# Kernel optimization log

Measured on AMD Instinct MI355X. Metric: run time of the kernel, lower is better.

## Reference

```python
import jax, jax.numpy as jnp
import numpy as np

REG_MAX = 16
NC = 80
TOPK = 10
ALPHA = 1.0
BETA = 6.0
BOX_W, CLS_W, DFL_W = 7.5, 0.5, 1.5
IMG = 1280.0


def _ciou(b1, b2, eps=1e-7):
    # b1, b2: [..., 4] xyxy, broadcastable
    b1x1, b1y1, b1x2, b1y2 = b1[..., 0], b1[..., 1], b1[..., 2], b1[..., 3]
    b2x1, b2y1, b2x2, b2y2 = b2[..., 0], b2[..., 1], b2[..., 2], b2[..., 3]
    w1, h1 = b1x2 - b1x1, b1y2 - b1y1
    w2, h2 = b2x2 - b2x1, b2y2 - b2y1
    inter = (jnp.maximum(jnp.minimum(b1x2, b2x2) - jnp.maximum(b1x1, b2x1), 0.0) *
             jnp.maximum(jnp.minimum(b1y2, b2y2) - jnp.maximum(b1y1, b2y1), 0.0))
    union = w1 * h1 + w2 * h2 - inter + eps
    iou = inter / union
    cw = jnp.maximum(b1x2, b2x2) - jnp.minimum(b1x1, b2x1)
    ch = jnp.maximum(b1y2, b2y2) - jnp.minimum(b1y1, b2y1)
    c2 = cw * cw + ch * ch + eps
    rho2 = ((b2x1 + b2x2 - b1x1 - b1x2) ** 2 + (b2y1 + b2y2 - b1y1 - b1y2) ** 2) / 4.0
    v = (4.0 / np.pi ** 2) * (jnp.arctan(w2 / (h2 + eps)) - jnp.arctan(w1 / (h1 + eps))) ** 2
    alpha = jax.lax.stop_gradient(v / (v - iou + (1.0 + eps)))
    return iou - (rho2 / c2 + v * alpha)


def _loss(p0, p1, p2, gt_boxes, gt_labels, strides):
    preds = [p0, p1, p2]
    B = p0.shape[0]
    aps, sts, pds, pcs = [], [], [], []
    for i, p in enumerate(preds):
        H, W = p.shape[2], p.shape[3]
        gy, gx = jnp.meshgrid(jnp.arange(H, dtype=p.dtype) + 0.5,
                              jnp.arange(W, dtype=p.dtype) + 0.5, indexing='ij')
        aps.append(jnp.stack([gx.ravel(), gy.ravel()], -1))          # [HW,2] feat units
        sts.append(jnp.ones((H * W, 1), p.dtype) * strides[i])       # [HW,1]
        pds.append(p[:, :4 * REG_MAX].reshape(B, 4, REG_MAX, H * W).transpose(0, 3, 1, 2))
        pcs.append(p[:, 4 * REG_MAX:].transpose(0, 2, 3, 1).reshape(B, H * W, NC))
    ap = jnp.concatenate(aps)                 # [N,2]
    st = jnp.concatenate(sts)                 # [N,1]
    pred_dist = jnp.concatenate(pds, axis=1)  # [B,N,4,R]
    pred_cls = jnp.concatenate(pcs, axis=1)   # [B,N,NC]
    proj = jnp.arange(REG_MAX, dtype=p0.dtype)
    M = gt_boxes.shape[1]
    N = ap.shape[0]

    def one_image(pd, pc, gb, gl):
        # decode boxes (image units)
        dist = jnp.einsum('nkr,r->nk', jax.nn.softmax(pd, -1), proj)        # [N,4]
        pred_boxes = jnp.concatenate([(ap - dist[:, :2]) * st,
                                      (ap + dist[:, 2:]) * st], -1)          # [N,4]
        # ---- TaskAlignedAssigner (no grad) ----
        sg = jax.lax.stop_gradient
        pb, ps, gbs = sg(pred_boxes), sg(jax.nn.sigmoid(pc)), sg(gb)
        ap_img = ap * st                                                     # [N,2]
        in_gt = ((ap_img[:, None, 0] >= gbs[None, :, 0]) & (ap_img[:, None, 0] <= gbs[None, :, 2]) &
                 (ap_img[:, None, 1] >= gbs[None, :, 1]) & (ap_img[:, None, 1] <= gbs[None, :, 3]))
        ious = jnp.maximum(_ciou(pb[:, None, :], gbs[None, :, :]), 0.0)      # [N,M]
        align = (ps[:, gl] ** ALPHA) * (ious ** BETA) * in_gt
        align = align / (align.max(0, keepdims=True) + 1e-9)
        align = align * (ious > 0.1)
        # topk anchors per GT; anchor takes the GT with max masked score
        #  sequential loop with strict '>' updates)
        vals, idx = jax.lax.top_k(align.T, TOPK)                             # [M,TOPK]
        masked = jnp.zeros((M, N), align.dtype).at[
            jnp.arange(M)[:, None], idx].set(jnp.where(vals > 0, vals, 0.0))
        col = masked.T                                                       # [N,M]
        best_gt = jnp.argmax(col, 1)
        best_score = col.max(1)
        fg = (best_score > 0).astype(pd.dtype)                               # [N]
        num_fg = jnp.maximum(fg.sum(), 1.0)
        labels = gl[best_gt]
        boxes = gbs[best_gt]
        # ---- box (CIoU) loss over fg ----
        box_loss = ((1.0 - _ciou(pred_boxes, boxes)) * fg).sum() / num_fg
        # ---- DFL loss over fg ----
        t = jnp.concatenate([ap - boxes[:, :2] / st, boxes[:, 2:] / st - ap], -1)
        t = jnp.clip(t, 0.0, REG_MAX - 1 - 0.01)   # box2dist clamp
        t = jnp.clip(t, 0.0, REG_MAX - 1e-4)       # DFLLoss clamp
        left = jnp.floor(t).astype(jnp.int32)
        right = jnp.minimum(left + 1, REG_MAX - 1)
        wl = right.astype(t.dtype) - t
        wr = t - left.astype(t.dtype)
        logp = jax.nn.log_softmax(pd, -1)                                    # [N,4,R]
        ce_l = -jnp.take_along_axis(logp, left[..., None], -1)[..., 0]
        ce_r = -jnp.take_along_axis(logp, right[..., None], -1)[..., 0]
        dfl_loss = ((ce_l * wl + ce_r * wr) * fg[:, None]).sum() / (num_fg * 4.0)
        # ---- cls BCE-with-logits over all anchors ----
        cls_t = jax.nn.one_hot(labels, NC, dtype=pc.dtype) * (best_score * fg)[:, None]
        cls_loss = (jnp.logaddexp(0.0, pc) - pc * cls_t).sum(1).mean()
        has_fg = (fg.sum() > 0).astype(pd.dtype)
        return box_loss * has_fg, cls_loss * has_fg, dfl_loss * has_fg

    bl, cl, dl = jax.vmap(one_image)(pred_dist, pred_cls, gt_boxes, gt_labels)
    return BOX_W * bl.sum() + CLS_W * cl.sum() + DFL_W * dl.sum()


def setup_inputs() -> dict:
    key = jax.random.key(0)
    ks = jax.random.split(key, 6)
    p0 = jax.random.normal(ks[0], (8, 144, 160, 160), jnp.float32)
    p1 = jax.random.normal(ks[1], (8, 144, 80, 80), jnp.float32)
    p2 = jax.random.normal(ks[2], (8, 144, 40, 40), jnp.float32)
    cxcy = jax.random.uniform(ks[3], (8, 32, 2), minval=64.0, maxval=IMG - 64.0)
    wh = jax.random.uniform(ks[4], (8, 32, 2), minval=16.0, maxval=256.0)
    gt_boxes = jnp.clip(jnp.concatenate([cxcy - wh / 2, cxcy + wh / 2], -1), 0.0, IMG)
    gt_labels = jax.random.randint(ks[5], (8, 32), 0, NC)
    strides = jnp.array([8.0, 16.0, 32.0], jnp.float32)
    return {"p0": p0, "p1": p1, "p2": p2, "gt_boxes": gt_boxes,
            "gt_labels": gt_labels, "strides": strides}


def reference(p0, p1, p2, gt_boxes, gt_labels, strides):
    return _loss(p0, p1, p2, gt_boxes, gt_labels, strides)
```

## Files before the change

### kernel.cpp

```cpp
#include <hip/hip_runtime.h>
#include <cstdint>

#define NANCHOR 33600
#define BATCH   8
#define MGT     32
#define NCLS    80
#define MAXFG   (BATCH * MGT * 10)

struct AInfo {
    const float* ch0;
    int   hw;
    float apx, apy, st;
};

__device__ __forceinline__ AInfo anchor_info(const float* p0, const float* p1,
                                             const float* p2, int b, int n) {
    AInfo r;
    if (n < 25600) {
        int nn = n;
        r.ch0 = p0 + (size_t)b * (144 * 25600) + nn;
        r.hw = 25600; r.st = 8.f;
        r.apx = (float)(nn % 160) + 0.5f;
        r.apy = (float)(nn / 160) + 0.5f;
    } else if (n < 32000) {
        int nn = n - 25600;
        r.ch0 = p1 + (size_t)b * (144 * 6400) + nn;
        r.hw = 6400; r.st = 16.f;
        r.apx = (float)(nn % 80) + 0.5f;
        r.apy = (float)(nn / 80) + 0.5f;
    } else {
        int nn = n - 32000;
        r.ch0 = p2 + (size_t)b * (144 * 1600) + nn;
        r.hw = 1600; r.st = 32.f;
        r.apx = (float)(nn % 40) + 0.5f;
        r.apy = (float)(nn / 40) + 0.5f;
    }
    return r;
}

__device__ __forceinline__ float ciou_f(float b1x1, float b1y1, float b1x2, float b1y2,
                                        float g1x, float g1y, float g2x, float g2y) {
    const float eps = 1e-7f;
    float w1 = b1x2 - b1x1, h1 = b1y2 - b1y1;
    float w2 = g2x - g1x,   h2 = g2y - g1y;
    float iw = fminf(b1x2, g2x) - fmaxf(b1x1, g1x);
    float ih = fminf(b1y2, g2y) - fmaxf(b1y1, g1y);
    float inter = fmaxf(iw, 0.f) * fmaxf(ih, 0.f);
    float uni = w1 * h1 + w2 * h2 - inter + eps;
    float iou = inter / uni;
    float cw = fmaxf(b1x2, g2x) - fminf(b1x1, g1x);
    float ch = fmaxf(b1y2, g2y) - fminf(b1y1, g1y);
    float c2 = cw * cw + ch * ch + eps;
    float dx = g1x + g2x - b1x1 - b1x2;
    float dy = g1y + g2y - b1y1 - b1y2;
    float rho2 = (dx * dx + dy * dy) * 0.25f;
    float t = atanf(w2 / (h2 + eps)) - atanf(w1 / (h1 + eps));
    float v = 0.40528473456935108577f * t * t;
    float alpha = v / (v - iou + (1.f + eps));
    return iou - (rho2 / c2 + v * alpha);
}

__device__ __forceinline__ float4 max4(float4 a, float4 b) {
    return make_float4(fmaxf(a.x, b.x), fmaxf(a.y, b.y), fmaxf(a.z, b.z), fmaxf(a.w, b.w));
}
__device__ __forceinline__ float fast_splus(float x) {
    return fmaxf(x, 0.f) + __logf(1.f + __expf(-fabsf(x)));
}


__global__ void k_init(float* acc) {
    acc[threadIdx.x] = 0.f;
}

__global__ __launch_bounds__(256) void k_decode(const float* __restrict__ p0,
                                                const float* __restrict__ p1,
                                                const float* __restrict__ p2,
                                                float4* __restrict__ px1,
                                                float4* __restrict__ py1,
                                                float4* __restrict__ px2,
                                                float4* __restrict__ py2,
                                                unsigned long long* __restrict__ best,
                                                float* __restrict__ acc) {
    int b = blockIdx.y;
    int role = blockIdx.z;
    int tid = threadIdx.x;

    if (role >= 4) {
        int sp_role = role - 4;
        const float4* pc0 = (const float4*)(p0 + (size_t)b * 3686400 + 1638400);
        const float4* pc1 = (const float4*)(p1 + (size_t)b * 921600  + 409600);
        const float4* pc2 = (const float4*)(p2 + (size_t)b * 230400  + 102400);
        float sp = 0.f;
        for (int g = (sp_role * 33 + blockIdx.x) * 256 + tid; g < 672000; g += 67584) {
            float4 x;
            if (g < 512000)      x = pc0[g];
            else if (g < 640000) x = pc1[g - 512000];
            else                 x = pc2[g - 640000];
            sp += fast_splus(x.x) + fast_splus(x.y) + fast_splus(x.z) + fast_splus(x.w);
        }
#pragma unroll
        for (int o = 32; o > 0; o >>= 1) sp += __shfl_down(sp, o, 64);
        if ((tid & 63) == 0) atomicAdd(&acc[64 + b * 8 + sp_role], sp);
        return;
    }

    int t = blockIdx.x * 256 + tid;
    if (t >= NANCHOR / 4) return;
    int n = t * 4;
    const float* ch0; int hw; float st, apx, apy;
    if (n < 25600) {
        ch0 = p0 + (size_t)b * (144 * 25600) + n;
        hw = 25600; st = 8.f;
        apx = (float)(n % 160) + 0.5f; apy = (float)(n / 160) + 0.5f;
    } else if (n < 32000) {
        int nn = n - 25600;
        ch0 = p1 + (size_t)b * (144 * 6400) + nn;
        hw = 6400; st = 16.f;
        apx = (float)(nn % 80) + 0.5f; apy = (float)(nn / 80) + 0.5f;
    } else {
        int nn = n - 32000;
        ch0 = p2 + (size_t)b * (144 * 1600) + nn;
        hw = 1600; st = 32.f;
        apx = (float)(nn % 40) + 0.5f; apy = (float)(nn / 40) + 0.5f;
    }

    const float* side = ch0 + (size_t)(role * 16) * hw;
    float4 v[16];
#pragma unroll
    for (int r = 0; r < 16; r++)
        v[r] = *(const float4*)(side + (size_t)r * hw);
    float4 mx = v[0];
#pragma unroll
    for (int r = 1; r < 16; r++) mx = max4(mx, v[r]);
    float4 s  = make_float4(0.f, 0.f, 0.f, 0.f);
    float4 sw = make_float4(0.f, 0.f, 0.f, 0.f);
#pragma unroll
    for (int r = 0; r < 16; r++) {
        float fr = (float)r;
        float ex = __expf(v[r].x - mx.x);
        float ey = __expf(v[r].y - mx.y);
        float ez = __expf(v[r].z - mx.z);
        float ew = __expf(v[r].w - mx.w);
        s.x += ex; s.y += ey; s.z += ez; s.w += ew;
        sw.x += ex * fr; sw.y += ey * fr; sw.z += ez * fr; sw.w += ew * fr;
    }
    float d0 = sw.x / s.x, d1 = sw.y / s.y, d2 = sw.z / s.z, d3 = sw.w / s.w;

    float4 res;
    if (role == 0)      res = make_float4((apx + 0.f - d0) * st, (apx + 1.f - d1) * st,
                                          (apx + 2.f - d2) * st, (apx + 3.f - d3) * st);
    else if (role == 1) res = make_float4((apy - d0) * st, (apy - d1) * st,
                                          (apy - d2) * st, (apy - d3) * st);
    else if (role == 2) res = make_float4((apx + 0.f + d0) * st, (apx + 1.f + d1) * st,
                                          (apx + 2.f + d2) * st, (apx + 3.f + d3) * st);
    else                res = make_float4((apy + d0) * st, (apy + d1) * st,
                                          (apy + d2) * st, (apy + d3) * st);

    size_t gi = ((size_t)b * NANCHOR + n) >> 2;
    float4* dst = (role == 0) ? px1 : (role == 1) ? py1 : (role == 2) ? px2 : py2;
    dst[gi] = res;

    if (role == 0) {
        ulonglong2* bq = (ulonglong2*)(best + (size_t)b * NANCHOR + n);
        bq[0] = make_ulonglong2(0ull, 0ull);
        bq[1] = make_ulonglong2(0ull, 0ull);
    }
}

__global__ __launch_bounds__(256) void k_assign(const float* __restrict__ p0,
                                                const float* __restrict__ p1,
                                                const float* __restrict__ p2,
                                                const float* __restrict__ px1,
                                                const float* __restrict__ py1,
                                                const float* __restrict__ px2,
                                                const float* __restrict__ py2,
                                                const float* __restrict__ gtb,
                                                const int* __restrict__ gtl,
                                                unsigned long long* __restrict__ best,
                                                float* __restrict__ acc,
                                                uint2* __restrict__ fglist) {
    int bm = blockIdx.x;
    int b = bm >> 5, m = bm & 31;
    const float* g = gtb + (size_t)(b * MGT + m) * 4;
    float g0 = g[0], g1 = g[1], g2 = g[2], g3 = g[3];
    int label = gtl[b * MGT + m];
    int tid = threadIdx.x;

    float tv[10];
    int   ti[10];
#pragma unroll
    for (int j = 0; j < 10; j++) { tv[j] = -1.f; ti[j] = 0x7fffffff; }
    float maxu = 0.f;

    const int   LW[3]   = {160, 80, 40};
    const int   LOFF[3] = {0, 25600, 32000};
    const float LST[3]  = {8.f, 16.f, 32.f};

    for (int l = 0; l < 3; l++) {
        float st = LST[l];
        int W = LW[l];
        float inv_st = 1.f / st;
        int ix0 = max(0,     (int)floorf(g0 * inv_st - 0.5f) - 1);
        int ix1 = min(W - 1, (int)ceilf (g2 * inv_st - 0.5f) + 1);
        int iy0 = max(0,     (int)floorf(g1 * inv_st - 0.5f) - 1);
        int iy1 = min(W - 1, (int)ceilf (g3 * inv_st - 0.5f) + 1);
        int nx = ix1 - ix0 + 1, ny = iy1 - iy0 + 1;
        if (nx <= 0 || ny <= 0) continue;
        int cnt = nx * ny;
        const float* lp = (l == 0) ? p0 : (l == 1) ? p1 : p2;
        int hw = W * W;
        const float* ch0 = lp + (size_t)b * 144 * hw;
        const float* pcls = ch0 + (size_t)(64 + label) * hw;

        for (int idx = tid; idx < cnt; idx += 256) {
            int iy = iy0 + idx / nx;
            int ix = ix0 + idx % nx;
            float ax = ((float)ix + 0.5f) * st;
            float ay = ((float)iy + 0.5f) * st;
            if (ax < g0 || ax > g2 || ay < g1 || ay > g3) continue;
            int nn = iy * W + ix;
            int n = LOFF[l] + nn;
            size_t bn = (size_t)b * NANCHOR + n;
            float c = ciou_f(px1[bn], py1[bn], px2[bn], py2[bn], g0, g1, g2, g3);
            float iou = fmaxf(c, 0.f);
            if (iou <= 0.f) continue;
            float pcv = pcls[nn];
            float ps = 1.f / (1.f + __expf(-pcv));
            float i2 = iou * iou;
            float a = ps * i2 * i2 * i2;
            maxu = fmaxf(maxu, a);
            if (iou > 0.1f && a > tv[9]) {
                tv[9] = a; ti[9] = n;
#pragma unroll
                for (int j = 9; j > 0; --j) {
                    if (tv[j] > tv[j - 1]) {
                        float tf = tv[j]; tv[j] = tv[j - 1]; tv[j - 1] = tf;
                        int   tt = ti[j]; ti[j] = ti[j - 1]; ti[j - 1] = tt;
                    }
                }
            }
        }
    }

    __shared__ float sval[2560];
    __shared__ int   sidx[2560];
    __shared__ float rv[256];
    __shared__ int   ra[256];
    __shared__ int   rs[256];
    __shared__ float smax[256];
    __shared__ int   winners[10];
    __shared__ int   nwin;

#pragma unroll
    for (int j = 0; j < 10; j++) {
        sval[tid * 10 + j] = tv[j];
        sidx[tid * 10 + j] = ti[j];
    }
    smax[tid] = maxu;
    if (tid == 0) nwin = 0;
    __syncthreads();
    for (int s = 128; s > 0; s >>= 1) {
        if (tid < s) smax[tid] = fmaxf(smax[tid], smax[tid + s]);
        __syncthreads();
    }
    float denom = smax[0] + 1e-9f;

    for (int r = 0; r < 10; r++) {
        float bv = -1.f; int ba = 0x7fffffff; int bs = -1;
#pragma unroll
        for (int j = 0; j < 10; j++) {
            int s0 = tid * 10 + j;
            float v = sval[s0]; int a0 = sidx[s0];
            if (v > bv || (v == bv && a0 < ba)) { bv = v; ba = a0; bs = s0; }
        }
        rv[tid] = bv; ra[tid] = ba; rs[tid] = bs;
        __syncthreads();
        for (int s = 128; s > 0; s >>= 1) {
            if (tid < s) {
                if (rv[tid + s] > rv[tid] ||
                    (rv[tid + s] == rv[tid] && ra[tid + s] < ra[tid])) {
                    rv[tid] = rv[tid + s]; ra[tid] = ra[tid + s]; rs[tid] = rs[tid + s];
                }
            }
            __syncthreads();
        }
        if (tid == 0 && rv[0] > 0.f) {
            float nv = rv[0] / denom;
            unsigned long long pk =
                ((unsigned long long)__float_as_uint(nv) << 32) |
                (unsigned long long)(31 - m);
            atomicMax(&best[(size_t)b * NANCHOR + ra[0]], pk);
            winners[nwin++] = ra[0];
            sval[rs[0]] = -1.f;
        }
        __syncthreads();
    }

    if (tid == 0 && nwin > 0) {
        unsigned int* list_cnt = (unsigned int*)(acc + 63);
        unsigned int base = atomicAdd(list_cnt, (unsigned int)nwin);
        for (int j = 0; j < nwin; j++)
            fglist[base + j] = make_uint2((unsigned int)(b * NANCHOR + winners[j]),
                                          (unsigned int)m);
    }
}

__global__ __launch_bounds__(256) void k_final(const float* __restrict__ p0,
                                               const float* __restrict__ p1,
                                               const float* __restrict__ p2,
                                               const float* __restrict__ px1,
                                               const float* __restrict__ py1,
                                               const float* __restrict__ px2,
                                               const float* __restrict__ py2,
                                               const float* __restrict__ gtb,
                                               const int* __restrict__ gtl,
                                               const unsigned long long* __restrict__ best,
                                               const uint2* __restrict__ fglist,
                                               float* __restrict__ acc) {
    __shared__ float sacc[BATCH][4];
    int tid = threadIdx.x;
    if (tid < BATCH * 4) sacc[tid >> 2][tid & 3] = 0.f;
    __syncthreads();

    unsigned int cnt = *(const unsigned int*)(acc + 63);
    unsigned int i = blockIdx.x * 256 + tid;
    if (i < cnt) {
        uint2 e = fglist[i];
        int bn = (int)e.x, m = (int)e.y;
        unsigned long long pk = best[bn];
        if ((unsigned int)(pk & 0xffffffffull) == (unsigned int)(31 - m)) {
            int b = bn / NANCHOR, n = bn % NANCHOR;
            float score = __uint_as_float((unsigned int)(pk >> 32));
            const float* g = gtb + (size_t)(b * MGT + m) * 4;
            float g0 = g[0], g1 = g[1], g2 = g[2], g3 = g[3];
            int label = gtl[b * MGT + m];
            float c = ciou_f(px1[bn], py1[bn], px2[bn], py2[bn], g0, g1, g2, g3);

            AInfo ai = anchor_info(p0, p1, p2, b, n);
            float inv_st = 1.f / ai.st;
            float t4[4] = { ai.apx - g0 * inv_st, ai.apy - g1 * inv_st,
                            g2 * inv_st - ai.apx, g3 * inv_st - ai.apy };
            float dfl = 0.f;
#pragma unroll
            for (int k = 0; k < 4; k++) {
                float t = fminf(fmaxf(t4[k], 0.f), 14.99f);
                int left = (int)floorf(t);
                int right = (left + 1 < 15) ? left + 1 : 15;
                float wl = (float)right - t;
                float wr = t - (float)left;
                float v[16];
                float mx = -1e30f;
#pragma unroll
                for (int r = 0; r < 16; r++) {
                    v[r] = ai.ch0[(size_t)(k * 16 + r) * ai.hw];
                    mx = fmaxf(mx, v[r]);
                }
                float s = 0.f;
#pragma unroll
                for (int r = 0; r < 16; r++) s += __expf(v[r] - mx);
                float lse = mx + __logf(s);
                dfl += (lse - v[left]) * wl + (lse - v[right]) * wr;
            }
            float pcv = ai.ch0[(size_t)(64 + label) * ai.hw];

            atomicAdd(&sacc[b][0], 1.f - c);
            atomicAdd(&sacc[b][1], dfl);
            atomicAdd(&sacc[b][2], pcv * score);
            atomicAdd(&sacc[b][3], 1.f);
        }
    }
    __syncthreads();
    if (tid < BATCH * 4) {
        float v = sacc[tid >> 2][tid & 3];
        if (v != 0.f) atomicAdd(&acc[(tid >> 2) * 8 + 1 + (tid & 3)], v);
    }
}

__global__ void k_combine(const float* __restrict__ acc, float* __restrict__ out) {
    if (blockIdx.x == 0 && threadIdx.x == 0) {
        float total = 0.f;
        for (int b = 0; b < BATCH; b++) {
            float sp = 0.f;
            for (int j = 0; j < 8; j++) sp += acc[64 + b * 8 + j];
            float nfr = acc[b * 8 + 4];
            float has = nfr > 0.f ? 1.f : 0.f;
            float nf = fmaxf(nfr, 1.f);
            float box_l = acc[b * 8 + 1] / nf;
            float cls_l = (sp - acc[b * 8 + 3]) / (float)NANCHOR;
            float dfl_l = acc[b * 8 + 2] / (nf * 4.f);
            total += has * (7.5f * box_l + 0.5f * cls_l + 1.5f * dfl_l);
        }
        out[0] = total;
    }
}

extern "C" void kernel_launch(void* const* d_in, const int* in_sizes, int n_in,
                              void* d_out, int out_size, void* d_ws, size_t ws_size,
                              hipStream_t stream) {
    (void)in_sizes; (void)n_in; (void)out_size; (void)ws_size;
    const float* p0  = (const float*)d_in[0];
    const float* p1  = (const float*)d_in[1];
    const float* p2  = (const float*)d_in[2];
    const float* gtb = (const float*)d_in[3];
    const int*   gtl = (const int*)d_in[4];

    const size_t BN = (size_t)BATCH * NANCHOR;
    char* ws = (char*)d_ws;
    unsigned long long* best = (unsigned long long*)ws;
    float* px1 = (float*)(ws + BN * 8);
    float* py1 = px1 + BN;
    float* px2 = py1 + BN;
    float* py2 = px2 + BN;
    float* acc = py2 + BN;
    uint2* fglist = (uint2*)(acc + 256);

    k_init   <<<1, 256, 0, stream>>>(acc);
    k_decode <<<dim3(33, BATCH, 12), 256, 0, stream>>>(p0, p1, p2,
                (float4*)px1, (float4*)py1, (float4*)px2, (float4*)py2, best, acc);
    k_assign <<<BATCH * MGT, 256, 0, stream>>>(p0, p1, p2, px1, py1, px2, py2,
                                               gtb, gtl, best, acc, fglist);
    k_final  <<<(MAXFG + 255) / 256, 256, 0, stream>>>(p0, p1, p2, px1, py1, px2, py2,
                                                       gtb, gtl, best, fglist, acc);
    k_combine<<<1, 64, 0, stream>>>(acc, (float*)d_out);
}
```

Measured before the change: 296.7 us.

## Flatten decode grid and give each softplus block a fixed contiguous chunk

The 3D decode grid becomes a 1D grid. Each decode thread now handles two box sides (x1/y1 or x2/y2) instead of one, which halves the decode blocks. The softplus blocks no longer use a strided grid loop; each one processes a fixed contiguous chunk of 25x256 float4 with a fully unrolled loop. The aim is better load balance and memory-level parallelism in the classification softplus sweep, at the cost of more register pressure in decode threads, which now hold two sets of 16 float4 values.

```diff
diff --git a/kernel.cpp b/kernel.cpp
--- a/kernel.cpp
+++ b/kernel.cpp
@@ -81,30 +81,37 @@
                                                 float4* __restrict__ py2,
                                                 unsigned long long* __restrict__ best,
                                                 float* __restrict__ acc) {
-    int b = blockIdx.y;
-    int role = blockIdx.z;
+    int bi = blockIdx.x;
     int tid = threadIdx.x;
 
-    if (role >= 4) {
-        int sp_role = role - 4;
-        const float4* pc0 = (const float4*)(p0 + (size_t)b * 3686400 + 1638400);
-        const float4* pc1 = (const float4*)(p1 + (size_t)b * 921600  + 409600);
-        const float4* pc2 = (const float4*)(p2 + (size_t)b * 230400  + 102400);
+    if (bi >= 528) {
+        int sbi = bi - 528;
+        int b = sbi / 105;
+        int r = sbi % 105;
+        const float4* base;
+        if (r < 80)
+            base = (const float4*)(p0 + (size_t)b * 3686400 + 1638400) + r * 6400;
+        else if (r < 100)
+            base = (const float4*)(p1 + (size_t)b * 921600 + 409600) + (r - 80) * 6400;
+        else
+            base = (const float4*)(p2 + (size_t)b * 230400 + 102400) + (r - 100) * 6400;
+
         float sp = 0.f;
-        for (int g = (sp_role * 33 + blockIdx.x) * 256 + tid; g < 672000; g += 67584) {
-            float4 x;
-            if (g < 512000)      x = pc0[g];
-            else if (g < 640000) x = pc1[g - 512000];
-            else                 x = pc2[g - 640000];
+#pragma unroll
+        for (int k = 0; k < 25; k++) {
+            float4 x = base[k * 256 + tid];
             sp += fast_splus(x.x) + fast_splus(x.y) + fast_splus(x.z) + fast_splus(x.w);
         }
 #pragma unroll
         for (int o = 32; o > 0; o >>= 1) sp += __shfl_down(sp, o, 64);
-        if ((tid & 63) == 0) atomicAdd(&acc[64 + b * 8 + sp_role], sp);
+        if ((tid & 63) == 0) atomicAdd(&acc[64 + b * 8 + (sbi & 7)], sp);
         return;
     }
 
-    int t = blockIdx.x * 256 + tid;
+    int b = bi / 66;
+    int rr = bi % 66;
+    int role = rr / 33;
+    int t = (rr % 33) * 256 + tid;
     if (t >= NANCHOR / 4) return;
     int n = t * 4;
     const float* ch0; int hw; float st, apx, apy;
@@ -124,46 +131,47 @@
         apx = (float)(nn % 40) + 0.5f; apy = (float)(nn / 40) + 0.5f;
     }
 
-    const float* side = ch0 + (size_t)(role * 16) * hw;
-    float4 v[16];
-#pragma unroll
-    for (int r = 0; r < 16; r++)
-        v[r] = *(const float4*)(side + (size_t)r * hw);
-    float4 mx = v[0];
-#pragma unroll
-    for (int r = 1; r < 16; r++) mx = max4(mx, v[r]);
-    float4 s  = make_float4(0.f, 0.f, 0.f, 0.f);
-    float4 sw = make_float4(0.f, 0.f, 0.f, 0.f);
-#pragma unroll
-    for (int r = 0; r < 16; r++) {
-        float fr = (float)r;
-        float ex = __expf(v[r].x - mx.x);
-        float ey = __expf(v[r].y - mx.y);
-        float ez = __expf(v[r].z - mx.z);
-        float ew = __expf(v[r].w - mx.w);
-        s.x += ex; s.y += ey; s.z += ez; s.w += ew;
-        sw.x += ex * fr; sw.y += ey * fr; sw.z += ez * fr; sw.w += ew * fr;
-    }
-    float d0 = sw.x / s.x, d1 = sw.y / s.y, d2 = sw.z / s.z, d3 = sw.w / s.w;
-
-    float4 res;
-    if (role == 0)      res = make_float4((apx + 0.f - d0) * st, (apx + 1.f - d1) * st,
-                                          (apx + 2.f - d2) * st, (apx + 3.f - d3) * st);
-    else if (role == 1) res = make_float4((apy - d0) * st, (apy - d1) * st,
-                                          (apy - d2) * st, (apy - d3) * st);
-    else if (role == 2) res = make_float4((apx + 0.f + d0) * st, (apx + 1.f + d1) * st,
-                                          (apx + 2.f + d2) * st, (apx + 3.f + d3) * st);
-    else                res = make_float4((apy + d0) * st, (apy + d1) * st,
-                                          (apy + d2) * st, (apy + d3) * st);
+    int k0 = role * 2;
+    float d[2][4];
+#pragma unroll
+    for (int kk = 0; kk < 2; kk++) {
+        float4 v[16];
+#pragma unroll
+        for (int r = 0; r < 16; r++)
+            v[r] = *(const float4*)(ch0 + (size_t)((k0 + kk) * 16 + r) * hw);
+        float4 mx = v[0];
+#pragma unroll
+        for (int r = 1; r < 16; r++) mx = max4(mx, v[r]);
+        float4 s  = make_float4(0.f, 0.f, 0.f, 0.f);
+        float4 sw = make_float4(0.f, 0.f, 0.f, 0.f);
+#pragma unroll
+        for (int r = 0; r < 16; r++) {
+            float fr = (float)r;
+            float ex = __expf(v[r].x - mx.x);
+            float ey = __expf(v[r].y - mx.y);
+            float ez = __expf(v[r].z - mx.z);
+            float ew = __expf(v[r].w - mx.w);
+            s.x += ex; s.y += ey; s.z += ez; s.w += ew;
+            sw.x += ex * fr; sw.y += ey * fr; sw.z += ez * fr; sw.w += ew * fr;
+        }
+        d[kk][0] = sw.x / s.x; d[kk][1] = sw.y / s.y;
+        d[kk][2] = sw.z / s.z; d[kk][3] = sw.w / s.w;
+    }
 
     size_t gi = ((size_t)b * NANCHOR + n) >> 2;
-    float4* dst = (role == 0) ? px1 : (role == 1) ? py1 : (role == 2) ? px2 : py2;
-    dst[gi] = res;
-
     if (role == 0) {
+        px1[gi] = make_float4((apx + 0.f - d[0][0]) * st, (apx + 1.f - d[0][1]) * st,
+                              (apx + 2.f - d[0][2]) * st, (apx + 3.f - d[0][3]) * st);
+        py1[gi] = make_float4((apy - d[1][0]) * st, (apy - d[1][1]) * st,
+                              (apy - d[1][2]) * st, (apy - d[1][3]) * st);
         ulonglong2* bq = (ulonglong2*)(best + (size_t)b * NANCHOR + n);
         bq[0] = make_ulonglong2(0ull, 0ull);
         bq[1] = make_ulonglong2(0ull, 0ull);
+    } else {
+        px2[gi] = make_float4((apx + 0.f + d[0][0]) * st, (apx + 1.f + d[0][1]) * st,
+                              (apx + 2.f + d[0][2]) * st, (apx + 3.f + d[0][3]) * st);
+        py2[gi] = make_float4((apy + d[1][0]) * st, (apy + d[1][1]) * st,
+                              (apy + d[1][2]) * st, (apy + d[1][3]) * st);
     }
 }
 
@@ -415,7 +423,7 @@
     uint2* fglist = (uint2*)(acc + 256);
 
     k_init   <<<1, 256, 0, stream>>>(acc);
-    k_decode <<<dim3(33, BATCH, 12), 256, 0, stream>>>(p0, p1, p2,
+    k_decode <<<528 + 840, 256, 0, stream>>>(p0, p1, p2,
                 (float4*)px1, (float4*)py1, (float4*)px2, (float4*)py2, best, acc);
     k_assign <<<BATCH * MGT, 256, 0, stream>>>(p0, p1, p2, px1, py1, px2, py2,
                                                gtb, gtl, best, acc, fglist);
```

Result: faster. 278.0 us (-6.3%).

## Stage decode and softplus inputs through LDS with global_load_lds and flat grid

Applied to the files above, without the earlier changes.

Rewrites k_decode to use a 1D grid of many small blocks. Each block copies its slice of the prediction tensor straight into shared memory with the global-to-LDS load builtin, then runs the DFL softmax decode or the softplus sum from LDS. This replaces per-thread strided float4 register loads with coalesced async copies into shared memory and gives far more blocks, aiming to raise memory-level parallelism on the bandwidth-bound pass. The cost is extra __syncthreads, 32KB of LDS per block (which limits occupancy), and scalar instead of float4 stores for the decoded planes.

```diff
diff --git a/kernel.cpp b/kernel.cpp
--- a/kernel.cpp
+++ b/kernel.cpp
@@ -60,11 +60,14 @@
     return iou - (rho2 / c2 + v * alpha);
 }
 
-__device__ __forceinline__ float4 max4(float4 a, float4 b) {
-    return make_float4(fmaxf(a.x, b.x), fmaxf(a.y, b.y), fmaxf(a.z, b.z), fmaxf(a.w, b.w));
-}
 __device__ __forceinline__ float fast_splus(float x) {
     return fmaxf(x, 0.f) + __logf(1.f + __expf(-fabsf(x)));
+}
+
+__device__ __forceinline__ void load16(const float* g, float* l) {
+    __builtin_amdgcn_global_load_lds(
+        (__attribute__((address_space(1))) void*)(g),
+        (__attribute__((address_space(3))) void*)(l), 16, 0, 0);
 }
 
 
@@ -75,96 +78,99 @@
 __global__ __launch_bounds__(256) void k_decode(const float* __restrict__ p0,
                                                 const float* __restrict__ p1,
                                                 const float* __restrict__ p2,
-                                                float4* __restrict__ px1,
-                                                float4* __restrict__ py1,
-                                                float4* __restrict__ px2,
-                                                float4* __restrict__ py2,
+                                                float* __restrict__ px1,
+                                                float* __restrict__ py1,
+                                                float* __restrict__ px2,
+                                                float* __restrict__ py2,
                                                 unsigned long long* __restrict__ best,
                                                 float* __restrict__ acc) {
-    int b = blockIdx.y;
-    int role = blockIdx.z;
+    __shared__ float lds[8192];
+    int bi = blockIdx.x;
     int tid = threadIdx.x;
-
-    if (role >= 4) {
-        int sp_role = role - 4;
-        const float4* pc0 = (const float4*)(p0 + (size_t)b * 3686400 + 1638400);
-        const float4* pc1 = (const float4*)(p1 + (size_t)b * 921600  + 409600);
-        const float4* pc2 = (const float4*)(p2 + (size_t)b * 230400  + 102400);
-        float sp = 0.f;
-        for (int g = (sp_role * 33 + blockIdx.x) * 256 + tid; g < 672000; g += 67584) {
-            float4 x;
-            if (g < 512000)      x = pc0[g];
-            else if (g < 640000) x = pc1[g - 512000];
-            else                 x = pc2[g - 640000];
-            sp += fast_splus(x.x) + fast_splus(x.y) + fast_splus(x.z) + fast_splus(x.w);
-        }
-#pragma unroll
-        for (int o = 32; o > 0; o >>= 1) sp += __shfl_down(sp, o, 64);
-        if ((tid & 63) == 0) atomicAdd(&acc[64 + b * 8 + sp_role], sp);
+    int w = tid >> 6, lane = tid & 63;
+
+    if (bi < 2144) {
+        int b = bi / 268;
+        int rem = bi % 268;
+        int s = rem / 67;
+        int ci = rem % 67;
+        const float* lp; int hw, loff, W, c; float st;
+        if (ci < 50)      { lp = p0 + (size_t)b * 3686400; hw = 25600; loff = 0;
+                            W = 160; st = 8.f;  c = ci; }
+        else if (ci < 63) { lp = p1 + (size_t)b * 921600;  hw = 6400;  loff = 25600;
+                            W = 80;  st = 16.f; c = ci - 50; }
+        else              { lp = p2 + (size_t)b * 230400;  hw = 1600;  loff = 32000;
+                            W = 40;  st = 32.f; c = ci - 63; }
+        const float* side = lp + (size_t)(s * 16) * hw;
+
+#pragma unroll
+        for (int i = 0; i < 8; i++) {
+            int seg = w * 8 + i;
+            int r = seg >> 1, h = seg & 1;
+            const float* g = side + (size_t)r * hw + c * 512 + h * 256 + lane * 4;
+            load16(g, lds + seg * 256);
+        }
+        __syncthreads();
+
+        float* plane = (s == 0) ? px1 : (s == 1) ? py1 : (s == 2) ? px2 : py2;
+#pragma unroll
+        for (int j = 0; j < 2; j++) {
+            int a = c * 512 + j * 256 + tid;
+            if (a >= hw) continue;
+            float v[16];
+            float mx = -1e30f;
+#pragma unroll
+            for (int r = 0; r < 16; r++) {
+                v[r] = lds[r * 512 + j * 256 + tid];
+                mx = fmaxf(mx, v[r]);
+            }
+            float sum = 0.f, sw = 0.f;
+#pragma unroll
+            for (int r = 0; r < 16; r++) {
+                float e = __expf(v[r] - mx);
+                sum += e;
+                sw += e * (float)r;
+            }
+            float d = sw / sum;
+            float ap = (s & 1) ? (float)(a / W) + 0.5f : (float)(a % W) + 0.5f;
+            float val = (s < 2) ? (ap - d) * st : (ap + d) * st;
+            size_t bn = (size_t)b * NANCHOR + loff + a;
+            plane[bn] = val;
+            if (s == 0) best[bn] = 0ull;
+        }
         return;
     }
 
-    int t = blockIdx.x * 256 + tid;
-    if (t >= NANCHOR / 4) return;
-    int n = t * 4;
-    const float* ch0; int hw; float st, apx, apy;
-    if (n < 25600) {
-        ch0 = p0 + (size_t)b * (144 * 25600) + n;
-        hw = 25600; st = 8.f;
-        apx = (float)(n % 160) + 0.5f; apy = (float)(n / 160) + 0.5f;
-    } else if (n < 32000) {
-        int nn = n - 25600;
-        ch0 = p1 + (size_t)b * (144 * 6400) + nn;
-        hw = 6400; st = 16.f;
-        apx = (float)(nn % 80) + 0.5f; apy = (float)(nn / 80) + 0.5f;
-    } else {
-        int nn = n - 32000;
-        ch0 = p2 + (size_t)b * (144 * 1600) + nn;
-        hw = 1600; st = 32.f;
-        apx = (float)(nn % 40) + 0.5f; apy = (float)(nn / 40) + 0.5f;
-    }
-
-    const float* side = ch0 + (size_t)(role * 16) * hw;
-    float4 v[16];
-#pragma unroll
-    for (int r = 0; r < 16; r++)
-        v[r] = *(const float4*)(side + (size_t)r * hw);
-    float4 mx = v[0];
-#pragma unroll
-    for (int r = 1; r < 16; r++) mx = max4(mx, v[r]);
-    float4 s  = make_float4(0.f, 0.f, 0.f, 0.f);
-    float4 sw = make_float4(0.f, 0.f, 0.f, 0.f);
-#pragma unroll
-    for (int r = 0; r < 16; r++) {
-        float fr = (float)r;
-        float ex = __expf(v[r].x - mx.x);
-        float ey = __expf(v[r].y - mx.y);
-        float ez = __expf(v[r].z - mx.z);
-        float ew = __expf(v[r].w - mx.w);
-        s.x += ex; s.y += ey; s.z += ez; s.w += ew;
-        sw.x += ex * fr; sw.y += ey * fr; sw.z += ez * fr; sw.w += ew * fr;
-    }
-    float d0 = sw.x / s.x, d1 = sw.y / s.y, d2 = sw.z / s.z, d3 = sw.w / s.w;
-
-    float4 res;
-    if (role == 0)      res = make_float4((apx + 0.f - d0) * st, (apx + 1.f - d1) * st,
-                                          (apx + 2.f - d2) * st, (apx + 3.f - d3) * st);
-    else if (role == 1) res = make_float4((apy - d0) * st, (apy - d1) * st,
-                                          (apy - d2) * st, (apy - d3) * st);
-    else if (role == 2) res = make_float4((apx + 0.f + d0) * st, (apx + 1.f + d1) * st,
-                                          (apx + 2.f + d2) * st, (apx + 3.f + d3) * st);
-    else                res = make_float4((apy + d0) * st, (apy + d1) * st,
-                                          (apy + d2) * st, (apy + d3) * st);
-
-    size_t gi = ((size_t)b * NANCHOR + n) >> 2;
-    float4* dst = (role == 0) ? px1 : (role == 1) ? py1 : (role == 2) ? px2 : py2;
-    dst[gi] = res;
-
-    if (role == 0) {
-        ulonglong2* bq = (ulonglong2*)(best + (size_t)b * NANCHOR + n);
-        bq[0] = make_ulonglong2(0ull, 0ull);
-        bq[1] = make_ulonglong2(0ull, 0ull);
-    }
+    int sbi = bi - 2144;
+    int b = sbi / 525;
+    int r = sbi % 525;
+    const float* base; int segbase;
+    if (r < 400)      { base = p0 + (size_t)b * 3686400 + 1638400; segbase = r * 20; }
+    else if (r < 500) { base = p1 + (size_t)b * 921600  + 409600;  segbase = (r - 400) * 20; }
+    else              { base = p2 + (size_t)b * 230400  + 102400;  segbase = (r - 500) * 20; }
+
+#pragma unroll
+    for (int i = 0; i < 5; i++) {
+        int seg = w * 5 + i;
+        const float* g = base + (size_t)(segbase + seg) * 256 + lane * 4;
+        load16(g, lds + seg * 256);
+    }
+    __syncthreads();
+
+    const float4* l4 = (const float4*)lds;
+    float sp = 0.f;
+#pragma unroll
+    for (int k = 0; k < 5; k++) {
+        float4 x = l4[k * 256 + tid];
+        sp += fast_splus(x.x) + fast_splus(x.y) + fast_splus(x.z) + fast_splus(x.w);
+    }
+#pragma unroll
+    for (int o = 32; o > 0; o >>= 1) sp += __shfl_down(sp, o, 64);
+    __syncthreads();
+    if (lane == 0) lds[w] = sp;
+    __syncthreads();
+    if (tid == 0)
+        atomicAdd(&acc[64 + b * 8 + (sbi & 7)], lds[0] + lds[1] + lds[2] + lds[3]);
 }
 
 __global__ __launch_bounds__(256) void k_assign(const float* __restrict__ p0,
@@ -415,8 +421,7 @@
     uint2* fglist = (uint2*)(acc + 256);
 
     k_init   <<<1, 256, 0, stream>>>(acc);
-    k_decode <<<dim3(33, BATCH, 12), 256, 0, stream>>>(p0, p1, p2,
-                (float4*)px1, (float4*)py1, (float4*)px2, (float4*)py2, best, acc);
+    k_decode <<<2144 + 4200, 256, 0, stream>>>(p0, p1, p2, px1, py1, px2, py2, best, acc);
     k_assign <<<BATCH * MGT, 256, 0, stream>>>(p0, p1, p2, px1, py1, px2, py2,
                                                gtb, gtl, best, acc, fglist);
     k_final  <<<(MAXFG + 255) / 256, 256, 0, stream>>>(p0, p1, p2, px1, py1, px2, py2,
```

Measured after the change: 263.4 us. -11.2%, faster.
